# Kernel optimization log

Hardware: AMD Instinct MI355X
Metric: run time of the kernel (lower is better)

## Reference

```python
import jax, jax.numpy as jnp
import numpy as np
import math

B, C, H, W = 16, 512, 32, 32
HEADS = 8
HD = C // HEADS            # 64 head_dim
NFREQ = HD // 4            # 16 (head_dim % 4 == 0)
MAX_FREQ = 128.0
T = H * W                  # 1024 tokens


def _make_so2_mat():
    # make_2dcoord: meshgrid('ij') of arange(H), arange(W) -> [H, W, 2]
    xg, yg = np.meshgrid(np.arange(H, dtype=np.float32), np.arange(W, dtype=np.float32), indexing='ij')
    coord = np.stack([xg, yg], -1)                                   # [H, W, 2]
    freqs = np.exp(np.linspace(0.0, math.log(MAX_FREQ), NFREQ)).astype(np.float32)  # [NFREQ]
    th = coord[..., None, :] * freqs[None, None, :, None]            # [H, W, NFREQ, 2]
    c, s = np.cos(th), np.sin(th)
    # rotation matrices [[c, -s], [s, c]] -> [H, W, NFREQ, 2(dim), 2, 2]
    mat = np.stack([np.stack([c, -s], -1), np.stack([s, c], -1)], -2)
    mat = mat.reshape(H * W, NFREQ * 2, 2, 2)                        # flatten(2,3) then flatten(0,1)
    return jnp.asarray(mat[:, : HD // 2])                            # [T, HD//2, 2, 2]


def setup_inputs() -> dict:
    key = jax.random.key(0)
    ks = jax.random.split(key, 5)
    mat = _make_so2_mat()
    return {
        'x': jax.random.normal(ks[0], (B, C, H, W), dtype=jnp.float32),
        'w_qkv': jax.random.normal(ks[1], (3 * C, C), dtype=jnp.float32) * 0.02,
        'b_qkv': jax.random.normal(ks[2], (3 * C,), dtype=jnp.float32) * 0.02,
        'w_o': jax.random.normal(ks[3], (C, C), dtype=jnp.float32) * 0.02,
        'b_o': jax.random.normal(ks[4], (C,), dtype=jnp.float32) * 0.02,
        'mat_q': mat,
        'mat_k': mat,
        'mat_v': mat,
        'mat_o': jnp.swapaxes(mat, -2, -1),
    }


def _rep_mul(rep, t):
    # rep: [T, HD//2, 2, 2]; t: [B, nh, T, HD] -> per-pair 2x2 rotation
    tb = t.reshape(B, HEADS, T, HD // 2, 2)
    return jnp.einsum('tfij,bntfj->bntfi', rep, tb).reshape(B, HEADS, T, HD)


def _split_heads(t):
    # 'b (c nh) h w -> b nh (h w) c' (c outer, nh inner in channel dim)
    return t.reshape(B, HD, HEADS, T).transpose(0, 2, 3, 1)


def reference(x, w_qkv, b_qkv, w_o, b_o, mat_q, mat_k, mat_v, mat_o):
    # 1x1 conv QKV projection == channel GEMM
    qkv = jnp.einsum('bchw,oc->bohw', x, w_qkv) + b_qkv[None, :, None, None]
    q, k, v = jnp.split(qkv, 3, axis=1)
    q, k, v = map(_split_heads, (q, k, v))                 # [B, nh, T, HD]
    q = _rep_mul(mat_q, q)
    k = _rep_mul(mat_k, k)
    v = _rep_mul(mat_v, v)
    scale = 1.0 / math.sqrt(HD)
    attn = jax.nn.softmax(jnp.einsum('bntd,bnsd->bnts', q, k) * scale, axis=-1)
    o = jnp.einsum('bnts,bnsd->bntd', attn, v)             # [B, nh, T, HD]
    o = _rep_mul(mat_o, o)
    # 'b nh (h w) c -> b (c nh) h w'
    o = o.reshape(B, HEADS, H, W, HD).transpose(0, 4, 1, 2, 3).reshape(B, C, H, W)
    return jnp.einsum('bchw,oc->bohw', o, w_o) + b_o[None, :, None, None]
```

## Files before the change

kernel.cpp:

```cpp
#include <hip/hip_runtime.h>


typedef __bf16 bf16x8 __attribute__((ext_vector_type(8)));
typedef __bf16 bf16x4 __attribute__((ext_vector_type(4)));
typedef float  f32x4  __attribute__((ext_vector_type(4)));
typedef unsigned int uint2_t __attribute__((ext_vector_type(2)));
typedef unsigned int uint4_t __attribute__((ext_vector_type(4)));

__device__ __forceinline__ f32x4 mfma16(bf16x8 a, bf16x8 b, f32x4 c) {
    return __builtin_amdgcn_mfma_f32_16x16x32_bf16(a, b, c, 0, 0, 0);
}

__device__ __forceinline__ void async16(const void* g, void* l) {
    __builtin_amdgcn_global_load_lds(
        (const __attribute__((address_space(1))) void*)g,
        (__attribute__((address_space(3))) void*)l, 16, 0, 0);
}

__device__ __forceinline__ unsigned int pack2(float a, float b) {
    unsigned short ua = __builtin_bit_cast(unsigned short, (__bf16)a);
    unsigned short ub = __builtin_bit_cast(unsigned short, (__bf16)b);
    return (unsigned int)ua | ((unsigned int)ub << 16);
}

__global__ void k_convert_w(const float* __restrict__ wq, const float* __restrict__ wo,
                            __bf16* __restrict__ wqb, __bf16* __restrict__ wob) {
    int i = blockIdx.x * 256 + threadIdx.x;
    if (i < 3 * 512 * 512) wqb[i] = (__bf16)wq[i];
    if (i < 512 * 512) {
        int o = i >> 9, k2 = i & 511;
        int nh = k2 >> 6, hd = k2 & 63;
        wob[i] = (__bf16)wo[o * 512 + hd * 8 + nh];
    }
}

__global__ void k_transpose_x(const float* __restrict__ x, __bf16* __restrict__ xt) {
    __shared__ float tile[64][65];
    const int b  = blockIdx.z;
    const int c0 = blockIdx.y * 64;
    const int t0 = blockIdx.x * 64;
    const int tx = threadIdx.x, ty = threadIdx.y;
    const float* xp = x + ((size_t)b * 512 + c0) * 1024 + t0;
#pragma unroll
    for (int j = 0; j < 16; j++)
        tile[ty + j * 4][tx] = xp[(ty + j * 4) * 1024 + tx];
    __syncthreads();
    __bf16* xo = xt + ((size_t)b * 1024 + t0) * 512 + c0;
#pragma unroll
    for (int j = 0; j < 16; j++)
        xo[(ty + j * 4) * 512 + tx] = (__bf16)tile[tx][ty + j * 4];
}

__global__ __launch_bounds__(512) void k_gemm_qkv(
        const __bf16* __restrict__ A, const __bf16* __restrict__ W,
        const float* __restrict__ bias,
        const float* __restrict__ matq, const float* __restrict__ matk,
        const float* __restrict__ matv,
        __bf16* __restrict__ qd, __bf16* __restrict__ kd, __bf16* __restrict__ vtd)
{
    __shared__ __bf16 As[2][256][64];
    __shared__ __bf16 Bs[2][256][64];
    const int tid = threadIdx.x;
    const int m0 = blockIdx.x * 256;
    const int jb = blockIdx.y;
    const int part = jb >> 1;
    const int nh_base = (jb & 1) * 4;
    const int lane = tid & 63, w = tid >> 6;
    const int ln = lane & 15, quad = lane >> 4;
    const int wr = w >> 2, wc = w & 3;

    const int srow = lane >> 3;
    const int scol = (((lane & 7) ^ srow) * 8);

    const __bf16* arow[4];
    const __bf16* brow[4];
#pragma unroll
    for (int jj = 0; jj < 4; jj++) {
        int rr = w * 32 + jj * 8 + srow;
        arow[jj] = &A[(size_t)(m0 + rr) * 512 + scol];
        int o = part * 512 + (rr & 63) * 8 + nh_base + (rr >> 6);
        brow[jj] = &W[(size_t)o * 512 + scol];
    }

    f32x4 acc[8][4] = {};

#define STAGE_QKV(T, BUF)                                                   \
    do {                                                                    \
        const int _k0 = (T) * 64;                                           \
        _Pragma("unroll")                                                   \
        for (int jj = 0; jj < 4; jj++)                                      \
            async16(arow[jj] + _k0, &As[BUF][w * 32 + jj * 8][0]);          \
        _Pragma("unroll")                                                   \
        for (int jj = 0; jj < 4; jj++)                                      \
            async16(brow[jj] + _k0, &Bs[BUF][w * 32 + jj * 8][0]);          \
    } while (0)

    STAGE_QKV(0, 0);
    STAGE_QKV(1, 1);
    asm volatile("s_waitcnt vmcnt(8)" ::: "memory");
    __builtin_amdgcn_s_barrier();

#pragma unroll
    for (int t = 0; t < 8; ++t) {
        const int cur = t & 1;
        bf16x8 af[2][8], wf[2][4];
#pragma unroll
        for (int h = 0; h < 2; h++) {
#pragma unroll
            for (int mi = 0; mi < 8; mi++)
                af[h][mi] = *(const bf16x8*)&As[cur][wr * 128 + mi * 16 + ln][(((h * 4 + quad) ^ (ln & 7)) * 8)];
#pragma unroll
            for (int ni = 0; ni < 4; ni++)
                wf[h][ni] = *(const bf16x8*)&Bs[cur][wc * 64 + ni * 16 + ln][(((h * 4 + quad) ^ (ln & 7)) * 8)];
        }
        asm volatile("s_waitcnt lgkmcnt(0)" ::: "memory");
        __builtin_amdgcn_sched_barrier(0);
        __builtin_amdgcn_s_barrier();
        if (t < 6) STAGE_QKV(t + 2, cur);
        __builtin_amdgcn_s_setprio(1);
#pragma unroll
        for (int h = 0; h < 2; h++)
#pragma unroll
            for (int mi = 0; mi < 8; mi++)
#pragma unroll
                for (int ni = 0; ni < 4; ni++)
                    acc[mi][ni] = mfma16(af[h][mi], wf[h][ni], acc[mi][ni]);
        __builtin_amdgcn_s_setprio(0);
        if (t < 6) { asm volatile("s_waitcnt vmcnt(8)" ::: "memory"); }
        else       { asm volatile("s_waitcnt vmcnt(0)" ::: "memory"); }
        __builtin_amdgcn_s_barrier();
    }
#undef STAGE_QKV

    const int nh = nh_base + wc;
    const int rowbase = m0 + wr * 128;
    const int b  = rowbase >> 10, t0 = rowbase & 1023;
    const int bh = b * 8 + nh;
    const int ip = ln & 1;
    const float2* matp = (const float2*)(part == 0 ? matq : (part == 1 ? matk : matv));
    __bf16* qkdst = (part == 0) ? qd : kd;
    const float qscale = (part == 0) ? 0.18033688011112042f : 1.0f;

#pragma unroll
    for (int ni = 0; ni < 4; ni++) {
        const int hd = ni * 16 + ln;
        const int f  = hd >> 1;
        const float bias_o = bias[part * 512 + hd * 8 + nh];
#pragma unroll
        for (int mi = 0; mi < 8; mi++) {
            const int tq = t0 + mi * 16 + quad * 4;
            if (part < 2) {
#pragma unroll
                for (int r = 0; r < 4; r++) {
                    int t = tq + r;
                    float val = acc[mi][ni][r] + bias_o;
                    float pr  = __shfl_xor(val, 1);
                    float2 mv = matp[((size_t)t * 32 + f) * 2 + ip];
                    float e  = ip ? pr : val;
                    float oo = ip ? val : pr;
                    float rv = (mv.x * e + mv.y * oo) * qscale;
                    qkdst[((size_t)bh * 1024 + t) * 64 + hd] = (__bf16)rv;
                }
            } else {
                __bf16 pack[4];
#pragma unroll
                for (int r = 0; r < 4; r++) {
                    int t = tq + r;
                    float val = acc[mi][ni][r] + bias_o;
                    float pr  = __shfl_xor(val, 1);
                    float2 mv = matp[((size_t)t * 32 + f) * 2 + ip];
                    float e  = ip ? pr : val;
                    float oo = ip ? val : pr;
                    pack[r] = (__bf16)(mv.x * e + mv.y * oo);
                }
                *(uint2*)&vtd[((size_t)bh * 64 + hd) * 1024 + tq] = *(const uint2*)pack;
            }
        }
    }
}

__global__ __launch_bounds__(512) void k_attn(
        const __bf16* __restrict__ q, const __bf16* __restrict__ kk,
        const __bf16* __restrict__ vt, const float* __restrict__ mato,
        __bf16* __restrict__ od)
{
    __shared__ __bf16 Ks[64][64];
    __shared__ __bf16 Vs[64][64];
    const int id = blockIdx.x;
    const int logical = (id >> 3) + (id & 7) * 64;
    const int bh = logical >> 2, qt = logical & 3;
    const int tid = threadIdx.x, w = tid >> 6, lane = tid & 63;
    const int ln = lane & 15, quad = lane >> 4;
    const int lx = ln & 7;
    const int srow = lane >> 3;
    const int scol = ((lane & 7) ^ srow) * 8;
    const int qr0 = qt * 256 + w * 32;

    bf16x8 qa[2][2];
#pragma unroll
    for (int mi = 0; mi < 2; mi++)
#pragma unroll
        for (int ki = 0; ki < 2; ki++)
            qa[mi][ki] = *(const bf16x8*)&q[((size_t)bh * 1024 + qr0 + mi * 16 + ln) * 64 + ki * 32 + quad * 8];

    const __bf16* kbase = kk + (size_t)bh * 1024 * 64;
    const __bf16* vbase = vt + (size_t)bh * 64 * 1024;

    f32x4 oacc[2][4] = {};
    f32x4 lacc[2] = {};

    bf16x8 ones;
#pragma unroll
    for (int j = 0; j < 8; j++) ones[j] = (__bf16)1.0f;

    for (int st = 0; st < 16; st++) {
        async16(kbase + (size_t)(st * 64 + w * 8 + srow) * 64 + scol, &Ks[w * 8][0]);
        async16(vbase + (size_t)(w * 8 + srow) * 1024 + st * 64 + scol, &Vs[w * 8][0]);
        __syncthreads();

        f32x4 sc[2][4] = {};
#pragma unroll
        for (int si = 0; si < 4; si++) {
            bf16x8 kb0 = *(const bf16x8*)&Ks[si * 16 + ln][((quad    ) ^ lx) * 8];
            bf16x8 kb1 = *(const bf16x8*)&Ks[si * 16 + ln][((quad + 4) ^ lx) * 8];
#pragma unroll
            for (int mi = 0; mi < 2; mi++) {
                sc[mi][si] = mfma16(kb0, qa[mi][0], sc[mi][si]);
                sc[mi][si] = mfma16(kb1, qa[mi][1], sc[mi][si]);
            }
        }

#pragma unroll
        for (int kt = 0; kt < 2; kt++) {
            bf16x8 pa[2];
#pragma unroll
            for (int mi = 0; mi < 2; mi++) {
                unsigned int u0 = pack2(exp2f(sc[mi][2 * kt][0]), exp2f(sc[mi][2 * kt][1]));
                unsigned int u1 = pack2(exp2f(sc[mi][2 * kt][2]), exp2f(sc[mi][2 * kt][3]));
                unsigned int v0 = pack2(exp2f(sc[mi][2 * kt + 1][0]), exp2f(sc[mi][2 * kt + 1][1]));
                unsigned int v1 = pack2(exp2f(sc[mi][2 * kt + 1][2]), exp2f(sc[mi][2 * kt + 1][3]));
                uint2_t r0 = __builtin_amdgcn_permlane32_swap(u0, v0, false, false);
                uint2_t r1 = __builtin_amdgcn_permlane32_swap(u1, v1, false, false);
                uint2_t s0 = __builtin_amdgcn_permlane16_swap(r0[0], r0[1], false, false);
                uint2_t s1 = __builtin_amdgcn_permlane16_swap(r1[0], r1[1], false, false);
                uint4_t pw;
                pw[0] = s0[0]; pw[1] = s1[0]; pw[2] = s0[1]; pw[3] = s1[1];
                pa[mi] = __builtin_bit_cast(bf16x8, pw);
            }
#pragma unroll
            for (int ni = 0; ni < 4; ni++) {
                bf16x8 vb = *(const bf16x8*)&Vs[ni * 16 + ln][((kt * 4 + quad) ^ lx) * 8];
                oacc[0][ni] = mfma16(vb, pa[0], oacc[0][ni]);
                oacc[1][ni] = mfma16(vb, pa[1], oacc[1][ni]);
            }
            lacc[0] = mfma16(ones, pa[0], lacc[0]);
            lacc[1] = mfma16(ones, pa[1], lacc[1]);
        }
        __syncthreads();
    }

    const float4* mo4 = (const float4*)mato;
#pragma unroll
    for (int mi = 0; mi < 2; mi++) {
        const int t = qr0 + mi * 16 + ln;
        const float invl = 1.0f / lacc[mi][0];
#pragma unroll
        for (int ni = 0; ni < 4; ni++) {
            const int hd0 = ni * 16 + quad * 4;
            const int f   = hd0 >> 1;
            float v0 = oacc[mi][ni][0] * invl;
            float v1 = oacc[mi][ni][1] * invl;
            float v2 = oacc[mi][ni][2] * invl;
            float v3 = oacc[mi][ni][3] * invl;
            float4 m1 = mo4[(size_t)t * 32 + f];
            float4 m2 = mo4[(size_t)t * 32 + f + 1];
            __bf16 pk[4];
            pk[0] = (__bf16)(m1.x * v0 + m1.y * v1);
            pk[1] = (__bf16)(m1.z * v0 + m1.w * v1);
            pk[2] = (__bf16)(m2.x * v2 + m2.y * v3);
            pk[3] = (__bf16)(m2.z * v2 + m2.w * v3);
            *(uint2*)&od[((size_t)bh * 1024 + t) * 64 + hd0] = *(const uint2*)pk;
        }
    }
}

__global__ __launch_bounds__(512) void k_gemm_out(
        const __bf16* __restrict__ A, const __bf16* __restrict__ W,
        const float* __restrict__ bias, float* __restrict__ out)
{
    __shared__ __bf16 As[2][128][64];
    __shared__ __bf16 Bs[2][256][64];
    const int tid = threadIdx.x;
    const int id = blockIdx.x;
    const int logical = (id >> 3) + (id & 7) * 32;
    const int m0 = (logical >> 1) * 128;
    const int n0 = (logical & 1) * 256;
    const int lane = tid & 63, w = tid >> 6;
    const int ln = lane & 15, quad = lane >> 4;
    const int wr = w >> 2, wc = w & 3;

    const int srow = lane >> 3;
    const int scol = (((lane & 7) ^ srow) * 8);

    const int bb = m0 >> 10, t00 = m0 & 1023;

    const __bf16* arow[2];
    const __bf16* brow[4];
#pragma unroll
    for (int jj = 0; jj < 2; jj++) {
        int rr = w * 16 + jj * 8 + srow;
        arow[jj] = &A[((size_t)bb * 8192 + t00 + rr) * 64 + scol];
    }
#pragma unroll
    for (int jj = 0; jj < 4; jj++) {
        int rr = w * 32 + jj * 8 + srow;
        brow[jj] = &W[(size_t)(n0 + rr) * 512 + scol];
    }

    f32x4 acc[4][4] = {};

#define STAGE_OUT(T, BUF)                                                   \
    do {                                                                    \
        const int _k0 = (T) * 64;                                           \
        _Pragma("unroll")                                                   \
        for (int jj = 0; jj < 2; jj++)                                      \
            async16(arow[jj] + (size_t)_k0 * 1024, &As[BUF][w * 16 + jj * 8][0]); \
        _Pragma("unroll")                                                   \
        for (int jj = 0; jj < 4; jj++)                                      \
            async16(brow[jj] + _k0, &Bs[BUF][w * 32 + jj * 8][0]);          \
    } while (0)

    STAGE_OUT(0, 0);
    STAGE_OUT(1, 1);
    asm volatile("s_waitcnt vmcnt(6)" ::: "memory");
    __builtin_amdgcn_s_barrier();

#pragma unroll
    for (int t = 0; t < 8; ++t) {
        const int cur = t & 1;
        bf16x8 af[2][4], wf[2][4];
#pragma unroll
        for (int h = 0; h < 2; h++) {
#pragma unroll
            for (int mi = 0; mi < 4; mi++)
                af[h][mi] = *(const bf16x8*)&As[cur][wr * 64 + mi * 16 + ln][(((h * 4 + quad) ^ (ln & 7)) * 8)];
#pragma unroll
            for (int ni = 0; ni < 4; ni++)
                wf[h][ni] = *(const bf16x8*)&Bs[cur][wc * 64 + ni * 16 + ln][(((h * 4 + quad) ^ (ln & 7)) * 8)];
        }
        asm volatile("s_waitcnt lgkmcnt(0)" ::: "memory");
        __builtin_amdgcn_sched_barrier(0);
        __builtin_amdgcn_s_barrier();
        if (t < 6) STAGE_OUT(t + 2, cur);
        __builtin_amdgcn_s_setprio(1);
#pragma unroll
        for (int h = 0; h < 2; h++)
#pragma unroll
            for (int mi = 0; mi < 4; mi++)
#pragma unroll
                for (int ni = 0; ni < 4; ni++)
                    acc[mi][ni] = mfma16(af[h][mi], wf[h][ni], acc[mi][ni]);
        __builtin_amdgcn_s_setprio(0);
        if (t < 6) { asm volatile("s_waitcnt vmcnt(6)" ::: "memory"); }
        else       { asm volatile("s_waitcnt vmcnt(0)" ::: "memory"); }
        __builtin_amdgcn_s_barrier();
    }
#undef STAGE_OUT

    const int rowbase = m0 + wr * 64;
    const int bb2 = rowbase >> 10, t0 = rowbase & 1023;
#pragma unroll
    for (int ni = 0; ni < 4; ni++) {
        int o = n0 + wc * 64 + ni * 16 + ln;
        float bias_o = bias[o];
#pragma unroll
        for (int mi = 0; mi < 4; mi++) {
            int t = t0 + mi * 16 + quad * 4;
            f32x4 v = acc[mi][ni];
            v[0] += bias_o; v[1] += bias_o; v[2] += bias_o; v[3] += bias_o;
            *(f32x4*)&out[((size_t)bb2 * 512 + o) * 1024 + t] = v;
        }
    }
}

extern "C" void kernel_launch(void* const* d_in, const int* in_sizes, int n_in,
                              void* d_out, int out_size, void* d_ws, size_t ws_size,
                              hipStream_t stream) {
    (void)in_sizes; (void)n_in; (void)out_size; (void)ws_size;
    const float* x     = (const float*)d_in[0];
    const float* w_qkv = (const float*)d_in[1];
    const float* b_qkv = (const float*)d_in[2];
    const float* w_o   = (const float*)d_in[3];
    const float* b_o   = (const float*)d_in[4];
    const float* mat_q = (const float*)d_in[5];
    const float* mat_k = (const float*)d_in[6];
    const float* mat_v = (const float*)d_in[7];
    const float* mat_o = (const float*)d_in[8];
    float* out = (float*)d_out;

    char* p = (char*)d_ws;
    __bf16* wqb = (__bf16*)p;  p += (size_t)3 * 512 * 512 * 2;
    __bf16* wob = (__bf16*)p;  p += (size_t)512 * 512 * 2;
    char* xt_base = p;
    __bf16* xt  = (__bf16*)p;  p += (size_t)16384 * 512 * 2;
    __bf16* qd  = (__bf16*)p;  p += (size_t)128 * 1024 * 64 * 2;
    __bf16* kd  = (__bf16*)p;  p += (size_t)128 * 1024 * 64 * 2;
    __bf16* vtd = (__bf16*)p;  p += (size_t)128 * 64 * 1024 * 2;
    __bf16* od  = (__bf16*)xt_base;

    k_convert_w  <<<dim3(3072),       dim3(256),    0, stream>>>(w_qkv, w_o, wqb, wob);
    k_transpose_x<<<dim3(16, 8, 16),  dim3(64, 4),  0, stream>>>(x, xt);
    k_gemm_qkv   <<<dim3(64, 6),      dim3(512),    0, stream>>>(xt, wqb, b_qkv, mat_q, mat_k, mat_v, qd, kd, vtd);
    k_attn       <<<dim3(512),        dim3(512),    0, stream>>>(qd, kd, vtd, mat_o, od);
    k_gemm_out   <<<dim3(256),        dim3(512),    0, stream>>>(od, wob, b_o, out);
}
```

Baseline: 237.1 us.

## Prepack QKV weights into MFMA fragment order and load B directly from global

The weight-conversion kernel now writes the QKV weights pre-swizzled into the exact per-lane MFMA fragment layout. The QKV GEMM then loads B fragments straight from global memory into registers, with no LDS staging. The M tile is halved to 128 rows and the grid doubled to improve occupancy. A is single-buffered in LDS with __syncthreads instead of the previous double-buffered async pipeline. The intent is to cut LDS traffic and footprint and add more blocks, at the risk of exposed global load latency for weights and less overlap on A.

```diff
diff --git a/kernel.cpp b/kernel.cpp
--- a/kernel.cpp
+++ b/kernel.cpp
@@ -24,9 +24,26 @@
 }
 
 __global__ void k_convert_w(const float* __restrict__ wq, const float* __restrict__ wo,
-                            __bf16* __restrict__ wqb, __bf16* __restrict__ wob) {
+                            __bf16* __restrict__ wqb2, __bf16* __restrict__ wob) {
     int i = blockIdx.x * 256 + threadIdx.x;
-    if (i < 3 * 512 * 512) wqb[i] = (__bf16)wq[i];
+    if (i < 3 * 512 * 512) {
+        int jb  = i >> 17;
+        int r   = i & 131071;
+        int t   = r >> 14;
+        int r2  = r & 16383;
+        int wc  = r2 >> 12;
+        int r3  = r2 & 4095;
+        int ni  = r3 >> 10;
+        int r4  = r3 & 1023;
+        int h   = r4 >> 9;
+        int r5  = r4 & 511;
+        int lane = r5 >> 3;
+        int e    = r5 & 7;
+        int quad = lane >> 4, ln = lane & 15;
+        int o = (jb >> 1) * 512 + (ni * 16 + ln) * 8 + (jb & 1) * 4 + wc;
+        int k = t * 64 + (h * 4 + quad) * 8 + e;
+        wqb2[i] = (__bf16)wq[o * 512 + k];
+    }
     if (i < 512 * 512) {
         int o = i >> 9, k2 = i & 511;
         int nh = k2 >> 6, hd = k2 & 63;
@@ -52,16 +69,15 @@
 }
 
 __global__ __launch_bounds__(512) void k_gemm_qkv(
-        const __bf16* __restrict__ A, const __bf16* __restrict__ W,
+        const __bf16* __restrict__ A, const __bf16* __restrict__ W2,
         const float* __restrict__ bias,
         const float* __restrict__ matq, const float* __restrict__ matk,
         const float* __restrict__ matv,
         __bf16* __restrict__ qd, __bf16* __restrict__ kd, __bf16* __restrict__ vtd)
 {
-    __shared__ __bf16 As[2][256][64];
-    __shared__ __bf16 Bs[2][256][64];
+    __shared__ __bf16 As[128][64];
     const int tid = threadIdx.x;
-    const int m0 = blockIdx.x * 256;
+    const int m0 = blockIdx.x * 128;
     const int jb = blockIdx.y;
     const int part = jb >> 1;
     const int nh_base = (jb & 1) * 4;
@@ -72,68 +88,55 @@
     const int srow = lane >> 3;
     const int scol = (((lane & 7) ^ srow) * 8);
 
-    const __bf16* arow[4];
-    const __bf16* brow[4];
-#pragma unroll
-    for (int jj = 0; jj < 4; jj++) {
-        int rr = w * 32 + jj * 8 + srow;
+    const __bf16* arow[2];
+#pragma unroll
+    for (int jj = 0; jj < 2; jj++) {
+        int rr = w * 16 + jj * 8 + srow;
         arow[jj] = &A[(size_t)(m0 + rr) * 512 + scol];
-        int o = part * 512 + (rr & 63) * 8 + nh_base + (rr >> 6);
-        brow[jj] = &W[(size_t)o * 512 + scol];
-    }
-
-    f32x4 acc[8][4] = {};
-
-#define STAGE_QKV(T, BUF)                                                   \
-    do {                                                                    \
-        const int _k0 = (T) * 64;                                           \
-        _Pragma("unroll")                                                   \
-        for (int jj = 0; jj < 4; jj++)                                      \
-            async16(arow[jj] + _k0, &As[BUF][w * 32 + jj * 8][0]);          \
-        _Pragma("unroll")                                                   \
-        for (int jj = 0; jj < 4; jj++)                                      \
-            async16(brow[jj] + _k0, &Bs[BUF][w * 32 + jj * 8][0]);          \
-    } while (0)
-
-    STAGE_QKV(0, 0);
-    STAGE_QKV(1, 1);
-    asm volatile("s_waitcnt vmcnt(8)" ::: "memory");
-    __builtin_amdgcn_s_barrier();
+    }
+    const __bf16* wbase = W2 + (size_t)jb * 131072 + wc * 4096 + lane * 8;
+
+    f32x4 acc[4][4] = {};
+
+#pragma unroll
+    for (int jj = 0; jj < 2; jj++)
+        async16(arow[jj], &As[w * 16 + jj * 8][0]);
+    __syncthreads();
 
 #pragma unroll
     for (int t = 0; t < 8; ++t) {
-        const int cur = t & 1;
-        bf16x8 af[2][8], wf[2][4];
-#pragma unroll
-        for (int h = 0; h < 2; h++) {
-#pragma unroll
-            for (int mi = 0; mi < 8; mi++)
-                af[h][mi] = *(const bf16x8*)&As[cur][wr * 128 + mi * 16 + ln][(((h * 4 + quad) ^ (ln & 7)) * 8)];
+        bf16x8 wf[2][4];
+#pragma unroll
+        for (int h = 0; h < 2; h++)
 #pragma unroll
             for (int ni = 0; ni < 4; ni++)
-                wf[h][ni] = *(const bf16x8*)&Bs[cur][wc * 64 + ni * 16 + ln][(((h * 4 + quad) ^ (ln & 7)) * 8)];
-        }
-        asm volatile("s_waitcnt lgkmcnt(0)" ::: "memory");
-        __builtin_amdgcn_sched_barrier(0);
-        __builtin_amdgcn_s_barrier();
-        if (t < 6) STAGE_QKV(t + 2, cur);
+                wf[h][ni] = *(const bf16x8*)(wbase + t * 16384 + ni * 1024 + h * 512);
+        bf16x8 af[2][4];
+#pragma unroll
+        for (int h = 0; h < 2; h++)
+#pragma unroll
+            for (int mi = 0; mi < 4; mi++)
+                af[h][mi] = *(const bf16x8*)&As[wr * 64 + mi * 16 + ln][(((h * 4 + quad) ^ (ln & 7)) * 8)];
+        __syncthreads();
+        if (t < 7) {
+#pragma unroll
+            for (int jj = 0; jj < 2; jj++)
+                async16(arow[jj] + (t + 1) * 64, &As[w * 16 + jj * 8][0]);
+        }
         __builtin_amdgcn_s_setprio(1);
 #pragma unroll
         for (int h = 0; h < 2; h++)
 #pragma unroll
-            for (int mi = 0; mi < 8; mi++)
+            for (int mi = 0; mi < 4; mi++)
 #pragma unroll
                 for (int ni = 0; ni < 4; ni++)
                     acc[mi][ni] = mfma16(af[h][mi], wf[h][ni], acc[mi][ni]);
         __builtin_amdgcn_s_setprio(0);
-        if (t < 6) { asm volatile("s_waitcnt vmcnt(8)" ::: "memory"); }
-        else       { asm volatile("s_waitcnt vmcnt(0)" ::: "memory"); }
-        __builtin_amdgcn_s_barrier();
-    }
-#undef STAGE_QKV
+        if (t < 7) __syncthreads();
+    }
 
     const int nh = nh_base + wc;
-    const int rowbase = m0 + wr * 128;
+    const int rowbase = m0 + wr * 64;
     const int b  = rowbase >> 10, t0 = rowbase & 1023;
     const int bh = b * 8 + nh;
     const int ip = ln & 1;
@@ -147,7 +150,7 @@
         const int f  = hd >> 1;
         const float bias_o = bias[part * 512 + hd * 8 + nh];
 #pragma unroll
-        for (int mi = 0; mi < 8; mi++) {
+        for (int mi = 0; mi < 4; mi++) {
             const int tq = t0 + mi * 16 + quad * 4;
             if (part < 2) {
 #pragma unroll
@@ -399,7 +402,7 @@
     float* out = (float*)d_out;
 
     char* p = (char*)d_ws;
-    __bf16* wqb = (__bf16*)p;  p += (size_t)3 * 512 * 512 * 2;
+    __bf16* wqb2 = (__bf16*)p; p += (size_t)3 * 512 * 512 * 2;
     __bf16* wob = (__bf16*)p;  p += (size_t)512 * 512 * 2;
     char* xt_base = p;
     __bf16* xt  = (__bf16*)p;  p += (size_t)16384 * 512 * 2;
@@ -408,9 +411,9 @@
     __bf16* vtd = (__bf16*)p;  p += (size_t)128 * 64 * 1024 * 2;
     __bf16* od  = (__bf16*)xt_base;
 
-    k_convert_w  <<<dim3(3072),       dim3(256),    0, stream>>>(w_qkv, w_o, wqb, wob);
+    k_convert_w  <<<dim3(3072),       dim3(256),    0, stream>>>(w_qkv, w_o, wqb2, wob);
     k_transpose_x<<<dim3(16, 8, 16),  dim3(64, 4),  0, stream>>>(x, xt);
-    k_gemm_qkv   <<<dim3(64, 6),      dim3(512),    0, stream>>>(xt, wqb, b_qkv, mat_q, mat_k, mat_v, qd, kd, vtd);
+    k_gemm_qkv   <<<dim3(128, 6),     dim3(512),    0, stream>>>(xt, wqb2, b_qkv, mat_q, mat_k, mat_v, qd, kd, vtd);
     k_attn       <<<dim3(512),        dim3(512),    0, stream>>>(qd, kd, vtd, mat_o, od);
     k_gemm_out   <<<dim3(256),        dim3(512),    0, stream>>>(od, wob, b_o, out);
 }
```

Result: no change. 236.3 us (-0.3%).
